# Kernel tuning notes

Hardware: AMD Instinct MI355X
Metric: run time of the kernel (lower is better)

Reference implementation:

```python
import jax, jax.numpy as jnp
import numpy as np

L = 4        # num decoder layers
H = 8        # heads
D = 512      # d_model
DFF = 2048   # ffn hidden
V = 8000     # target vocab
B = 16       # batch
S_ENC = 128  # encoder seq len
T = 32       # decode target_length
START, END, NULL = 1, 2, 0
NEG = -1e9
EPS = 1e-6


def sinusoid_pos(max_len, d):
    pos = np.arange(max_len)[:, None].astype(np.float32)
    i = np.arange(d)[None, :].astype(np.float32)
    ang = pos / np.power(10000.0, (2.0 * np.floor(i / 2.0)) / d)
    pe = np.where(np.arange(d)[None, :] % 2 == 0, np.sin(ang), np.cos(ang))
    return jnp.asarray(pe[None], jnp.float32)  # [1, max_len, d]


def setup_inputs() -> dict:
    key = jax.random.key(0)
    ks = jax.random.split(key, 16)
    g = lambda k, shape: jax.random.normal(k, shape, jnp.float32) * 0.02
    return {
        "target_length": T,
        "encoder_output": jax.random.normal(ks[0], (B, S_ENC, D), jnp.float32),
        "padding_mask": jnp.zeros((B, S_ENC), jnp.float32),  # 1.0 where padded
        "embed": g(ks[1], (V, D)),
        "wq": g(ks[2], (L, D, D)), "wk": g(ks[3], (L, D, D)),
        "wv": g(ks[4], (L, D, D)), "wo": g(ks[5], (L, D, D)),
        "cwq": g(ks[6], (L, D, D)), "cwk": g(ks[7], (L, D, D)),
        "cwv": g(ks[8], (L, D, D)), "cwo": g(ks[9], (L, D, D)),
        "w1": g(ks[10], (L, D, DFF)), "b1": jnp.zeros((L, DFF), jnp.float32),
        "w2": g(ks[11], (L, DFF, D)), "b2": jnp.zeros((L, D), jnp.float32),
        "ln_g": jnp.ones((L, 3, D), jnp.float32), "ln_b": jnp.zeros((L, 3, D), jnp.float32),
        "fc_w": g(ks[12], (D, V)), "fc_b": jnp.zeros((V,), jnp.float32),
    }


def ln(x, g, b):
    m = jnp.mean(x, axis=-1, keepdims=True)
    v = jnp.mean(jnp.square(x - m), axis=-1, keepdims=True)
    return (x - m) * jax.lax.rsqrt(v + EPS) * g + b


def mha(q_in, kv_in, wq, wk, wv, wo, mask):
    Bn, Sq, d = q_in.shape
    dh = d // H
    q = (q_in @ wq).reshape(Bn, Sq, H, dh)
    k = (kv_in @ wk).reshape(Bn, -1, H, dh)
    v = (kv_in @ wv).reshape(Bn, -1, H, dh)
    s = jnp.einsum('bqhd,bkhd->bhqk', q, k) / jnp.sqrt(jnp.float32(dh)) + mask
    a = jax.nn.softmax(s, axis=-1)
    o = jnp.einsum('bhqk,bkhd->bqhd', a, v).reshape(Bn, Sq, d)
    return o @ wo


def decoder_stack(x, encoder_output, self_mask, cross_mask,
                  wq, wk, wv, wo, cwq, cwk, cwv, cwo,
                  w1, b1, w2, b2, ln_g, ln_b):
    for i in range(L):
        a = mha(x, x, wq[i], wk[i], wv[i], wo[i], self_mask)
        x = ln(x + a, ln_g[i, 0], ln_b[i, 0])
        a2 = mha(x, encoder_output, cwq[i], cwk[i], cwv[i], cwo[i], cross_mask)
        x = ln(x + a2, ln_g[i, 1], ln_b[i, 1])
        f = jax.nn.relu(x @ w1[i] + b1[i]) @ w2[i] + b2[i]
        x = ln(x + f, ln_g[i, 2], ln_b[i, 2])
    return x


def reference(target_length, encoder_output, padding_mask, embed,
              wq, wk, wv, wo, cwq, cwk, cwv, cwo,
              w1, b1, w2, b2, ln_g, ln_b, fc_w, fc_b):
    Bn, S, d = encoder_output.shape
    Tp1 = target_length + 1
    pos_enc = sinusoid_pos(Tp1, d)
    sqrt_d = jnp.sqrt(jnp.float32(d))
    cross_mask = padding_mask[:, None, None, :] * NEG  # [B,1,1,S_enc]
    tokens0 = jnp.full((Bn, Tp1), NULL, jnp.int32).at[:, 0].set(START)
    done0 = jnp.zeros((Bn,), bool)

    def step(carry, t):
        tokens, done = carry
        # re-embed the whole (fixed-size, masked) prefix buffer each step
        x = embed[tokens] * sqrt_d + pos_enc
        # only positions <= t are valid keys; no look-ahead mask (matches original)
        self_mask = jnp.where(jnp.arange(Tp1) <= t, 0.0, NEG)[None, None, None, :]
        x = decoder_stack(x, encoder_output, self_mask, cross_mask,
                          wq, wk, wv, wo, cwq, cwk, cwv, cwo,
                          w1, b1, w2, b2, ln_g, ln_b)
        out = x[:, t, :] @ fc_w + fc_b  # logits at last valid position
        max_idx = jnp.argmax(out, axis=-1).astype(jnp.int32)
        done = done | (max_idx == END)
        tok = jnp.where(done, jnp.int32(NULL), max_idx)
        tokens = tokens.at[:, t + 1].set(tok)
        return (tokens, done), None

    (tokens, done), _ = jax.lax.scan(step, (tokens0, done0), jnp.arange(target_length))
    return tokens[:, 1:].astype(jnp.int64)
```

## Files before the change

kernel.cpp:

```cpp
#include <hip/hip_runtime.h>
#include <math.h>

#define L_   4
#define H_   8
#define D_   512
#define DH   64
#define DFF_ 2048
#define V_   8000
#define B_   16
#define SENC 128
#define T_   32
#define TP1  33
#define NEGV -1e9f
#define EPSV 1e-6f
#define SQRTD 22.627416997969522f
#define XSZ  ((size_t)TP1 * B_ * D_)

__global__ __launch_bounds__(256) void gemm32_k(
    const float* __restrict__ A, const float* __restrict__ W,
    const float* __restrict__ bias, float* __restrict__ C,
    int M, int N, int K, int kchunk, size_t pstride, int relu, int tmode)
{
    __shared__ __align__(16) float As[2][16][34];
    __shared__ __align__(16) float Bs[2][16][68];
    int tid = threadIdx.x;
    int tx = tid & 15, ty = tid >> 4;
    int m0 = blockIdx.y * 32, n0 = blockIdx.x * 64;
    int kbeg = blockIdx.z * kchunk;
    int niter = kchunk >> 4;
    C += (size_t)blockIdx.z * pstride;
    int am = tid >> 2, aseg = tid & 3;
    int bk = tid >> 4, bc4 = (tid & 15) * 4;
    float4 aReg = make_float4(0.f, 0.f, 0.f, 0.f), bReg;
    {
        int k0 = kbeg;
        if (tid < 128) {
            int gm = m0 + am;
            if (gm < M) aReg = *(const float4*)&A[(size_t)gm * K + k0 + aseg * 4];
        }
        bReg = *(const float4*)&W[(size_t)(k0 + bk) * N + n0 + bc4];
    }
    if (tid < 128) {
        As[0][aseg * 4 + 0][am] = aReg.x;
        As[0][aseg * 4 + 1][am] = aReg.y;
        As[0][aseg * 4 + 2][am] = aReg.z;
        As[0][aseg * 4 + 3][am] = aReg.w;
    }
    *(float4*)&Bs[0][bk][bc4] = bReg;
    __syncthreads();
    float acc[2][4] = {};
    for (int it = 0; it < niter; it++) {
        int cur = it & 1;
        if (it + 1 < niter) {
            int k0 = kbeg + (it + 1) * 16;
            if (tid < 128) {
                int gm = m0 + am;
                aReg = make_float4(0.f, 0.f, 0.f, 0.f);
                if (gm < M) aReg = *(const float4*)&A[(size_t)gm * K + k0 + aseg * 4];
            }
            bReg = *(const float4*)&W[(size_t)(k0 + bk) * N + n0 + bc4];
        }
        #pragma unroll
        for (int kk = 0; kk < 16; kk++) {
            float2 a2 = *(const float2*)&As[cur][kk][ty * 2];
            float4 b4 = *(const float4*)&Bs[cur][kk][tx * 4];
            acc[0][0] += a2.x * b4.x; acc[0][1] += a2.x * b4.y;
            acc[0][2] += a2.x * b4.z; acc[0][3] += a2.x * b4.w;
            acc[1][0] += a2.y * b4.x; acc[1][1] += a2.y * b4.y;
            acc[1][2] += a2.y * b4.z; acc[1][3] += a2.y * b4.w;
        }
        if (it + 1 < niter) {
            int nxt = 1 - cur;
            if (tid < 128) {
                As[nxt][aseg * 4 + 0][am] = aReg.x;
                As[nxt][aseg * 4 + 1][am] = aReg.y;
                As[nxt][aseg * 4 + 2][am] = aReg.z;
                As[nxt][aseg * 4 + 3][am] = aReg.w;
            }
            *(float4*)&Bs[nxt][bk][bc4] = bReg;
        }
        __syncthreads();
    }
    #pragma unroll
    for (int i = 0; i < 2; i++) {
        int gm = m0 + ty * 2 + i;
        if (gm >= M) continue;
        #pragma unroll
        for (int j = 0; j < 4; j++) {
            int gn = n0 + tx * 4 + j;
            float vv = acc[i][j];
            if (bias) vv += bias[gn];
            if (relu) vv = fmaxf(vv, 0.f);
            if (tmode == 1)
                C[(size_t)(gm >> 7) * 65536 + (size_t)gn * SENC + (gm & 127)] = vv;
            else
                C[(size_t)gm * N + gn] = vv;
        }
    }
}

__global__ __launch_bounds__(256) void gemm_qkv_k(
    const float* __restrict__ A, const float* __restrict__ W0,
    const float* __restrict__ W1, const float* __restrict__ W2,
    float* __restrict__ Cb, int M)
{
    __shared__ __align__(16) float As[2][16][34];
    __shared__ __align__(16) float Bs[2][16][68];
    int sel = blockIdx.x >> 3;
    const float* W = (sel == 0) ? W0 : ((sel == 1) ? W1 : W2);
    float* C = Cb + (size_t)sel * XSZ;
    int tid = threadIdx.x;
    int tx = tid & 15, ty = tid >> 4;
    int m0 = blockIdx.y * 32, n0 = (blockIdx.x & 7) * 64;
    int am = tid >> 2, aseg = tid & 3;
    int bk = tid >> 4, bc4 = (tid & 15) * 4;
    float4 aReg = make_float4(0.f, 0.f, 0.f, 0.f), bReg;
    {
        if (tid < 128) {
            int gm = m0 + am;
            if (gm < M) aReg = *(const float4*)&A[(size_t)gm * D_ + aseg * 4];
        }
        bReg = *(const float4*)&W[(size_t)bk * D_ + n0 + bc4];
    }
    if (tid < 128) {
        As[0][aseg * 4 + 0][am] = aReg.x;
        As[0][aseg * 4 + 1][am] = aReg.y;
        As[0][aseg * 4 + 2][am] = aReg.z;
        As[0][aseg * 4 + 3][am] = aReg.w;
    }
    *(float4*)&Bs[0][bk][bc4] = bReg;
    __syncthreads();
    float acc[2][4] = {};
    for (int it = 0; it < 32; it++) {
        int cur = it & 1;
        if (it + 1 < 32) {
            int k0 = (it + 1) * 16;
            if (tid < 128) {
                int gm = m0 + am;
                aReg = make_float4(0.f, 0.f, 0.f, 0.f);
                if (gm < M) aReg = *(const float4*)&A[(size_t)gm * D_ + k0 + aseg * 4];
            }
            bReg = *(const float4*)&W[(size_t)(k0 + bk) * D_ + n0 + bc4];
        }
        #pragma unroll
        for (int kk = 0; kk < 16; kk++) {
            float2 a2 = *(const float2*)&As[cur][kk][ty * 2];
            float4 b4 = *(const float4*)&Bs[cur][kk][tx * 4];
            acc[0][0] += a2.x * b4.x; acc[0][1] += a2.x * b4.y;
            acc[0][2] += a2.x * b4.z; acc[0][3] += a2.x * b4.w;
            acc[1][0] += a2.y * b4.x; acc[1][1] += a2.y * b4.y;
            acc[1][2] += a2.y * b4.z; acc[1][3] += a2.y * b4.w;
        }
        if (it + 1 < 32) {
            int nxt = 1 - cur;
            if (tid < 128) {
                As[nxt][aseg * 4 + 0][am] = aReg.x;
                As[nxt][aseg * 4 + 1][am] = aReg.y;
                As[nxt][aseg * 4 + 2][am] = aReg.z;
                As[nxt][aseg * 4 + 3][am] = aReg.w;
            }
            *(float4*)&Bs[nxt][bk][bc4] = bReg;
        }
        __syncthreads();
    }
    #pragma unroll
    for (int i = 0; i < 2; i++) {
        int gm = m0 + ty * 2 + i;
        if (gm >= M) continue;
        #pragma unroll
        for (int j = 0; j < 4; j++) {
            int gn = n0 + tx * 4 + j;
            if (sel == 1)
                C[(size_t)(gm & 15) * 16896 + (size_t)gn * TP1 + (gm >> 4)] =
                    acc[i][j];
            else
                C[(size_t)gm * D_ + gn] = acc[i][j];
        }
    }
}

__global__ void init_k(int* __restrict__ tokens, int* __restrict__ done,
                       float* __restrict__ cmask, const float* __restrict__ pm)
{
    int tid = threadIdx.x + blockIdx.x * 256;
    if (tid < B_ * TP1) tokens[tid] = ((tid % TP1) == 0) ? 1 : 0;
    if (tid < B_) done[tid] = 0;
    if (tid < B_ * SENC) cmask[tid] = pm[tid] * NEGV;
}

__global__ __launch_bounds__(256) void pe_k(float* __restrict__ pe)
{
    int p = blockIdx.x;
    for (int d = threadIdx.x; d < D_; d += 256) {
        float fd = (float)(2 * (d / 2)) / (float)D_;
        float ang = (float)p / powf(10000.f, fd);
        pe[(size_t)p * D_ + d] = (d & 1) ? cosf(ang) : sinf(ang);
    }
}

__global__ __launch_bounds__(256) void embed_k(
    const float* __restrict__ embed, int* __restrict__ tokens,
    float* __restrict__ x, const float* __restrict__ pe,
    const float* __restrict__ cand_v, const int* __restrict__ cand_i,
    int* __restrict__ done, int t)
{
    int p = blockIdx.x;
    int b = blockIdx.y;
    int tid = threadIdx.x;
    __shared__ float sv[128];
    __shared__ int si[128];
    __shared__ int stok;
    if (p == t && t > 0) {
        if (tid < 128) {
            float val = -1e30f; int idx = 0x7fffffff;
            if (tid < 125) {
                val = cand_v[(size_t)b * 125 + tid];
                idx = cand_i[(size_t)b * 125 + tid];
            }
            sv[tid] = val; si[tid] = idx;
        }
        __syncthreads();
        for (int s = 64; s; s >>= 1) {
            if (tid < s) {
                float ov = sv[tid + s]; int oi = si[tid + s];
                if (ov > sv[tid] || (ov == sv[tid] && oi < si[tid])) {
                    sv[tid] = ov; si[tid] = oi;
                }
            }
            __syncthreads();
        }
        if (tid == 0) {
            int best = si[0];
            int dn = done[b] | (best == 2 ? 1 : 0);
            done[b] = dn;
            int tk = dn ? 0 : best;
            tokens[b * TP1 + t] = tk;
            stok = tk;
        }
        __syncthreads();
    }
    int tok = (p == t && t > 0) ? stok : tokens[b * TP1 + p];
    const float* e = embed + (size_t)tok * D_;
    const float* pr = pe + (size_t)p * D_;
    float* xr = x + ((size_t)p * B_ + b) * D_;
    int c0 = tid * 2;
    float2 ev = *(const float2*)&e[c0];
    float2 pv = *(const float2*)&pr[c0];
    float2 o;
    o.x = ev.x * SQRTD + pv.x;
    o.y = ev.y * SQRTD + pv.y;
    *(float2*)&xr[c0] = o;
}

__device__ __forceinline__ float block_sum(float s) {
    __shared__ float red[4];
    #pragma unroll
    for (int off = 32; off; off >>= 1) s += __shfl_xor(s, off);
    if ((threadIdx.x & 63) == 0) red[threadIdx.x >> 6] = s;
    __syncthreads();
    float tot = red[0] + red[1] + red[2] + red[3];
    __syncthreads();
    return tot;
}

__device__ __forceinline__ float4 block_sum4(float4 s) {
    __shared__ __align__(16) float red4[4][4];
    #pragma unroll
    for (int off = 32; off; off >>= 1) {
        s.x += __shfl_xor(s.x, off);
        s.y += __shfl_xor(s.y, off);
        s.z += __shfl_xor(s.z, off);
        s.w += __shfl_xor(s.w, off);
    }
    if ((threadIdx.x & 63) == 0) *(float4*)red4[threadIdx.x >> 6] = s;
    __syncthreads();
    float4 t;
    t.x = red4[0][0] + red4[1][0] + red4[2][0] + red4[3][0];
    t.y = red4[0][1] + red4[1][1] + red4[2][1] + red4[3][1];
    t.z = red4[0][2] + red4[1][2] + red4[2][2] + red4[3][2];
    t.w = red4[0][3] + red4[1][3] + red4[2][3] + red4[3][3];
    __syncthreads();
    return t;
}

__global__ __launch_bounds__(256) void attn_mega_k(
    const float* __restrict__ q, const float* __restrict__ kT,
    const float* __restrict__ v, const float* __restrict__ wo,
    const float* __restrict__ KcT, const float* __restrict__ Vc,
    const float* __restrict__ cmask, const float* __restrict__ cwq,
    const float* __restrict__ cwo, float* __restrict__ x,
    const float* __restrict__ lg, const float* __restrict__ lb, int P)
{
    int b = blockIdx.x;
    int p0 = blockIdx.y * 4;
    int tid = threadIdx.x;
    int c0 = tid * 2;
    __shared__ float xs[4][D_];
    __shared__ float arow[4][D_];
    __shared__ float scs[4][H_][SENC + 4];
    __shared__ float inv[4][H_];
    #pragma unroll
    for (int g = 0; g < 4; g++) {
        float2 qv = make_float2(0.f, 0.f);
        if (p0 + g < P)
            qv = *(const float2*)&q[((size_t)(p0 + g) * B_ + b) * D_ + c0];
        *(float2*)&arow[g][c0] = qv;
    }
    __syncthreads();
    {
        int h = tid >> 5, kp = tid & 31;
        float a0 = 0.f, a1 = 0.f, a2 = 0.f, a3 = 0.f;
        if (kp < P) {
            const float* kb = kT + ((size_t)(b * 8 + h) * 64) * TP1 + kp;
            #pragma unroll 8
            for (int d = 0; d < 64; d++) {
                float kv = kb[(size_t)d * TP1];
                a0 += arow[0][h * 64 + d] * kv;
                a1 += arow[1][h * 64 + d] * kv;
                a2 += arow[2][h * 64 + d] * kv;
                a3 += arow[3][h * 64 + d] * kv;
            }
        }
        scs[0][h][kp] = a0 * 0.125f;
        scs[1][h][kp] = a1 * 0.125f;
        scs[2][h][kp] = a2 * 0.125f;
        scs[3][h][kp] = a3 * 0.125f;
    }
    __syncthreads();
    {
        int gh = tid >> 3, lane8 = tid & 7;
        int g = gh >> 3, h = gh & 7;
        float mx = -1e30f;
        for (int j = lane8; j < P; j += 8) mx = fmaxf(mx, scs[g][h][j]);
        mx = fmaxf(mx, __shfl_xor(mx, 1));
        mx = fmaxf(mx, __shfl_xor(mx, 2));
        mx = fmaxf(mx, __shfl_xor(mx, 4));
        float sum = 0.f;
        for (int j = lane8; j < P; j += 8) {
            float e = expf(scs[g][h][j] - mx);
            scs[g][h][j] = e;
            sum += e;
        }
        sum += __shfl_xor(sum, 1);
        sum += __shfl_xor(sum, 2);
        sum += __shfl_xor(sum, 4);
        if (lane8 == 0) inv[g][h] = 1.f / sum;
    }
    __syncthreads();
    {
        int h = tid >> 5;
        float o0[4] = {0.f, 0.f, 0.f, 0.f}, o1[4] = {0.f, 0.f, 0.f, 0.f};
        for (int j = 0; j < P; j++) {
            float2 vv = *(const float2*)&v[((size_t)j * B_ + b) * D_ + c0];
            #pragma unroll
            for (int g = 0; g < 4; g++) {
                float w = scs[g][h][j];
                o0[g] += w * vv.x; o1[g] += w * vv.y;
            }
        }
        #pragma unroll
        for (int g = 0; g < 4; g++) {
            arow[g][c0]     = o0[g] * inv[g][h];
            arow[g][c0 + 1] = o1[g] * inv[g][h];
        }
    }
    __syncthreads();
    {
        float v0[4], v1[4];
        #pragma unroll
        for (int g = 0; g < 4; g++) {
            float2 xv = make_float2(0.f, 0.f);
            if (p0 + g < P)
                xv = *(const float2*)&x[((size_t)(p0 + g) * B_ + b) * D_ + c0];
            v0[g] = xv.x; v1[g] = xv.y;
        }
        #pragma unroll 8
        for (int k = 0; k < D_; k++) {
            float2 wv = *(const float2*)&wo[(size_t)k * D_ + c0];
            #pragma unroll
            for (int g = 0; g < 4; g++) {
                float a = arow[g][k];
                v0[g] += a * wv.x; v1[g] += a * wv.y;
            }
// ... 65 lines not shown
    __syncthreads();
    {
        int gh = tid >> 3, lane8 = tid & 7;
        int g = gh >> 3, h = gh & 7;
        float mx = -1e30f;
        for (int s = lane8; s < SENC; s += 8) mx = fmaxf(mx, scs[g][h][s]);
        mx = fmaxf(mx, __shfl_xor(mx, 1));
        mx = fmaxf(mx, __shfl_xor(mx, 2));
        mx = fmaxf(mx, __shfl_xor(mx, 4));
        float sum = 0.f;
        for (int s = lane8; s < SENC; s += 8) {
            float e = expf(scs[g][h][s] - mx);
            scs[g][h][s] = e;
            sum += e;
        }
        sum += __shfl_xor(sum, 1);
        sum += __shfl_xor(sum, 2);
        sum += __shfl_xor(sum, 4);
        if (lane8 == 0) inv[g][h] = 1.f / sum;
    }
    __syncthreads();
    {
        int h = tid >> 5;
        float o0[4] = {0.f, 0.f, 0.f, 0.f}, o1[4] = {0.f, 0.f, 0.f, 0.f};
        for (int s = 0; s < SENC; s++) {
            float2 vv = *(const float2*)&Vc[((size_t)b * SENC + s) * D_ + c0];
            #pragma unroll
            for (int g = 0; g < 4; g++) {
                float w = scs[g][h][s];
                o0[g] += w * vv.x; o1[g] += w * vv.y;
            }
        }
        #pragma unroll
        for (int g = 0; g < 4; g++) {
            arow[g][c0]     = o0[g] * inv[g][h];
            arow[g][c0 + 1] = o1[g] * inv[g][h];
        }
    }
    __syncthreads();
    {
        float v0[4], v1[4];
        #pragma unroll
        for (int g = 0; g < 4; g++) {
            v0[g] = xs[g][c0]; v1[g] = xs[g][c0 + 1];
        }
        #pragma unroll 8
        for (int k = 0; k < D_; k++) {
            float2 wv = *(const float2*)&cwo[(size_t)k * D_ + c0];
            #pragma unroll
            for (int g = 0; g < 4; g++) {
                float a = arow[g][k];
                v0[g] += a * wv.x; v1[g] += a * wv.y;
            }
        }
        float4 s1 = make_float4(v0[0] + v1[0], v0[1] + v1[1],
                                v0[2] + v1[2], v0[3] + v1[3]);
        float4 m4 = block_sum4(s1);
        float mean[4] = {m4.x * (1.f / 512.f), m4.y * (1.f / 512.f),
                         m4.z * (1.f / 512.f), m4.w * (1.f / 512.f)};
        float d0[4], d1[4];
        #pragma unroll
        for (int g = 0; g < 4; g++) {
            d0[g] = v0[g] - mean[g]; d1[g] = v1[g] - mean[g];
        }
        float4 s2 = make_float4(d0[0] * d0[0] + d1[0] * d1[0],
                                d0[1] * d0[1] + d1[1] * d1[1],
                                d0[2] * d0[2] + d1[2] * d1[2],
                                d0[3] * d0[3] + d1[3] * d1[3]);
        float4 w4 = block_sum4(s2);
        float var[4] = {w4.x * (1.f / 512.f), w4.y * (1.f / 512.f),
                        w4.z * (1.f / 512.f), w4.w * (1.f / 512.f)};
        float g0 = lg[D_ + c0], g1 = lg[D_ + c0 + 1];
        float bb0 = lb[D_ + c0], bb1 = lb[D_ + c0 + 1];
        #pragma unroll
        for (int g = 0; g < 4; g++) {
            if (p0 + g < P) {
                float rs = rsqrtf(var[g] + EPSV);
                float* xr = x + ((size_t)(p0 + g) * B_ + b) * D_;
                xr[c0]     = d0[g] * rs * g0 + bb0;
                xr[c0 + 1] = d1[g] * rs * g1 + bb1;
            }
        }
    }
}

__global__ __launch_bounds__(256) void ln_red_k(
    float* __restrict__ x, const float* __restrict__ parts, size_t pstride,
    int nparts, const float* __restrict__ bias,
    const float* __restrict__ gam, const float* __restrict__ bet)
{
    int r = blockIdx.x;
    float* xr = x + (size_t)r * D_;
    int tid = threadIdx.x;
    float v0 = xr[tid];
    float v1 = xr[tid + 256];
    for (int s = 0; s < nparts; s++) {
        const float* pr = parts + (size_t)s * pstride + (size_t)r * D_;
        v0 += pr[tid];
        v1 += pr[tid + 256];
    }
    if (bias) { v0 += bias[tid]; v1 += bias[tid + 256]; }
    float mean = block_sum(v0 + v1) * (1.f / 512.f);
    float d0 = v0 - mean, d1 = v1 - mean;
    float var = block_sum(d0 * d0 + d1 * d1) * (1.f / 512.f);
    float rs = rsqrtf(var + EPSV);
    xr[tid]       = d0 * rs * gam[tid] + bet[tid];
    xr[tid + 256] = d1 * rs * gam[tid + 256] + bet[tid + 256];
}

__global__ __launch_bounds__(256) void logits_k(
    const float* __restrict__ x, const float* __restrict__ fcw,
    const float* __restrict__ fcb, float* __restrict__ cand_v,
    int* __restrict__ cand_i, int t)
{
    __shared__ float xs[B_][D_];
    __shared__ float red[4][64][B_];
    int tid = threadIdx.x;
    for (int i = tid; i < B_ * D_; i += 256) {
        int b = i >> 9, d = i & 511;
        xs[b][d] = x[((size_t)t * B_ + b) * D_ + d];
    }
    __syncthreads();
    int lane = tid & 63, ks = tid >> 6;
    int col = blockIdx.x * 64 + lane;
    float acc[B_] = {};
    int kb = ks * 128;
    for (int k = kb; k < kb + 128; k++) {
        float w = fcw[(size_t)k * V_ + col];
        #pragma unroll
        for (int b = 0; b < B_; b++) acc[b] += xs[b][k] * w;
    }
    #pragma unroll
    for (int b = 0; b < B_; b++) red[ks][lane][b] = acc[b];
    __syncthreads();
    if (ks == 0) {
        float bias = fcb[col];
        #pragma unroll
        for (int b = 0; b < B_; b++) {
            float val = red[0][lane][b] + red[1][lane][b]
                      + red[2][lane][b] + red[3][lane][b] + bias;
            int idx = col;
            #pragma unroll
            for (int off = 32; off; off >>= 1) {
                float ov = __shfl_down(val, off);
                int oi = __shfl_down(idx, off);
                if (ov > val || (ov == val && oi < idx)) { val = ov; idx = oi; }
            }
            if (lane == 0) {
                cand_v[(size_t)b * 125 + blockIdx.x] = val;
                cand_i[(size_t)b * 125 + blockIdx.x] = idx;
            }
        }
    }
}

__global__ __launch_bounds__(128) void writeout_k(
    const int* __restrict__ tokens, const float* __restrict__ cand_v,
    const int* __restrict__ cand_i, const int* __restrict__ done,
    int* __restrict__ out)
{
    int b = blockIdx.x;
    int tid = threadIdx.x;
    __shared__ float sv[128];
    __shared__ int si[128];
    __shared__ int stok;
    float val = -1e30f; int idx = 0x7fffffff;
    if (tid < 125) {
        val = cand_v[(size_t)b * 125 + tid];
        idx = cand_i[(size_t)b * 125 + tid];
    }
    sv[tid] = val; si[tid] = idx;
    __syncthreads();
    for (int s = 64; s; s >>= 1) {
        if (tid < s) {
            float ov = sv[tid + s]; int oi = si[tid + s];
            if (ov > sv[tid] || (ov == sv[tid] && oi < si[tid])) {
                sv[tid] = ov; si[tid] = oi;
            }
        }
        __syncthreads();
    }
    if (tid == 0) {
        int best = si[0];
        int dn = done[b] | (best == 2 ? 1 : 0);
        stok = dn ? 0 : best;
    }
    __syncthreads();
    if (tid < T_)
        out[b * T_ + tid] = (tid == T_ - 1) ? stok : tokens[b * TP1 + tid + 1];
}

extern "C" void kernel_launch(void* const* d_in, const int* in_sizes, int n_in,
                              void* d_out, int out_size, void* d_ws, size_t ws_size,
                              hipStream_t stream)
{
    const float* enc   = (const float*)d_in[1];
    const float* pm    = (const float*)d_in[2];
    const float* embed = (const float*)d_in[3];
    const float* wq    = (const float*)d_in[4];
    const float* wk    = (const float*)d_in[5];
    const float* wv    = (const float*)d_in[6];
    const float* wo    = (const float*)d_in[7];
    const float* cwq   = (const float*)d_in[8];
    const float* cwk   = (const float*)d_in[9];
    const float* cwv   = (const float*)d_in[10];
    const float* cwo   = (const float*)d_in[11];
    const float* w1    = (const float*)d_in[12];
    const float* b1    = (const float*)d_in[13];
    const float* w2    = (const float*)d_in[14];
    const float* b2    = (const float*)d_in[15];
    const float* ln_g  = (const float*)d_in[16];
    const float* ln_b  = (const float*)d_in[17];
    const float* fcw   = (const float*)d_in[18];
    const float* fcb   = (const float*)d_in[19];

    float* ws = (float*)d_ws;
    size_t off = 0;
    float* x     = ws + off; off += XSZ;
    float* qkv   = ws + off; off += 3 * XSZ;
    float* parts = ws + off; off += 4 * XSZ;
    float* ffnh  = ws + off; off += (size_t)TP1 * B_ * DFF_;
    float* cand_v= ws + off; off += (size_t)B_ * 125;
    float* KcT   = ws + off; off += (size_t)L_ * B_ * SENC * D_;
    float* Vc    = ws + off; off += (size_t)L_ * B_ * SENC * D_;
    float* cmask = ws + off; off += (size_t)B_ * SENC;
    float* pe    = ws + off; off += (size_t)TP1 * D_;
    int* cand_i  = (int*)(ws + off); off += (size_t)B_ * 125;
    int* tokens  = (int*)(ws + off); off += (B_ * TP1 + 63) & ~63;
    int* done    = (int*)(ws + off); off += 64;

    init_k<<<8, 256, 0, stream>>>(tokens, done, cmask, pm);
    pe_k<<<TP1, 256, 0, stream>>>(pe);

    const size_t KVL = (size_t)B_ * SENC * D_;
    for (int l = 0; l < L_; l++) {
        gemm32_k<<<dim3(8, (B_ * SENC) / 32), 256, 0, stream>>>(
            enc, cwk + (size_t)l * D_ * D_, nullptr, KcT + l * KVL,
            B_ * SENC, D_, D_, D_, 0, 0, 1);
        gemm32_k<<<dim3(8, (B_ * SENC) / 32), 256, 0, stream>>>(
            enc, cwv + (size_t)l * D_ * D_, nullptr, Vc + l * KVL,
            B_ * SENC, D_, D_, D_, 0, 0, 0);
    }

    for (int t = 0; t < T_; t++) {
        int P = t + 1;
        int M = P * B_;
        int mt = (M + 31) / 32;

        embed_k<<<dim3(P, B_), 256, 0, stream>>>(
            embed, tokens, x, pe, cand_v, cand_i, done, t);

        for (int l = 0; l < L_; l++) {
            const size_t lw = (size_t)l * D_ * D_;
            gemm_qkv_k<<<dim3(24, mt), 256, 0, stream>>>(
                x, wq + lw, wk + lw, wv + lw, qkv, M);
            attn_mega_k<<<dim3(B_, (P + 3) / 4), 256, 0, stream>>>(
                qkv, qkv + XSZ, qkv + 2 * XSZ, wo + lw,
                KcT + l * KVL, Vc + l * KVL, cmask, cwq + lw, cwo + lw, x,
                ln_g + (size_t)(l * 3 + 0) * D_, ln_b + (size_t)(l * 3 + 0) * D_, P);
            gemm32_k<<<dim3(32, mt), 256, 0, stream>>>(
                x, w1 + (size_t)l * D_ * DFF_, b1 + (size_t)l * DFF_, ffnh,
                M, DFF_, D_, D_, 0, 1, 0);
            gemm32_k<<<dim3(8, mt, 4), 256, 0, stream>>>(
                ffnh, w2 + (size_t)l * DFF_ * D_, nullptr, parts,
                M, D_, DFF_, 512, XSZ, 0, 0);
            ln_red_k<<<M, 256, 0, stream>>>(x, parts, XSZ, 4, b2 + (size_t)l * D_,
                ln_g + (size_t)(l * 3 + 2) * D_, ln_b + (size_t)(l * 3 + 2) * D_);
        }

        logits_k<<<V_ / 64, 256, 0, stream>>>(x, fcw, fcb, cand_v, cand_i, t);
    }

    writeout_k<<<B_, 128, 0, stream>>>(tokens, cand_v, cand_i, done, (int*)d_out);
}
```

Before: 24.24 ms.

## Fuse whole decode loop into one persistent cooperative kernel with grid barriers

Replaces the roughly 800 separate kernel launches (embed, qkv, attention, FFN, layernorm, logits per step and layer) with a single persistent cooperative kernel of 256 blocks. The blocks loop over the same tiles and separate stages with an atomic-counter grid barrier. The goal is to remove launch overhead and inter-kernel gaps, which dominate because each step has small M. The cost is a spin barrier per stage and 48KB of static shared memory per block, which may limit occupancy. If the cooperative launch fails, the original multi-kernel path is kept as a fallback.

Result: slower. 84.92 ms (+250.3%).

```diff
diff --git a/kernel.cpp b/kernel.cpp
--- a/kernel.cpp
+++ b/kernel.cpp
@@ -15,20 +15,69 @@
 #define EPSV 1e-6f
 #define SQRTD 22.627416997969522f
 #define XSZ  ((size_t)TP1 * B_ * D_)
-
-__global__ __launch_bounds__(256) void gemm32_k(
+#define NB   256
+
+__device__ __forceinline__ float block_sum(float s) {
+    __shared__ float red[4];
+    #pragma unroll
+    for (int off = 32; off; off >>= 1) s += __shfl_xor(s, off);
+    if ((threadIdx.x & 63) == 0) red[threadIdx.x >> 6] = s;
+    __syncthreads();
+    float tot = red[0] + red[1] + red[2] + red[3];
+    __syncthreads();
+    return tot;
+}
+
+__device__ __forceinline__ float4 block_sum4(float4 s) {
+    __shared__ __align__(16) float red4[4][4];
+    #pragma unroll
+    for (int off = 32; off; off >>= 1) {
+        s.x += __shfl_xor(s.x, off);
+        s.y += __shfl_xor(s.y, off);
+        s.z += __shfl_xor(s.z, off);
+        s.w += __shfl_xor(s.w, off);
+    }
+    if ((threadIdx.x & 63) == 0) *(float4*)red4[threadIdx.x >> 6] = s;
+    __syncthreads();
+    float4 t;
+    t.x = red4[0][0] + red4[1][0] + red4[2][0] + red4[3][0];
+    t.y = red4[0][1] + red4[1][1] + red4[2][1] + red4[3][1];
+    t.z = red4[0][2] + red4[1][2] + red4[2][2] + red4[3][2];
+    t.w = red4[0][3] + red4[1][3] + red4[2][3] + red4[3][3];
+    __syncthreads();
+    return t;
+}
+
+__device__ __forceinline__ void gsync(unsigned* bar, unsigned& gen)
+{
+    __syncthreads();
+    if (threadIdx.x == 0) {
+        __threadfence();
+        atomicAdd(bar, 1u);
+        gen += NB;
+        while (__hip_atomic_load(bar, __ATOMIC_RELAXED,
+                                 __HIP_MEMORY_SCOPE_AGENT) < gen)
+            __builtin_amdgcn_s_sleep(4);
+        __threadfence();
+    }
+    __syncthreads();
+}
+
+
+__device__ void gemm_tile(
     const float* __restrict__ A, const float* __restrict__ W,
     const float* __restrict__ bias, float* __restrict__ C,
-    int M, int N, int K, int kchunk, size_t pstride, int relu, int tmode)
-{
-    __shared__ __align__(16) float As[2][16][34];
-    __shared__ __align__(16) float Bs[2][16][68];
+    int M, int N, int K, int kchunk, size_t pstride, int relu, int tmode,
+    int bx, int by, int bz, float* smem)
+{
+    float (*As)[16][34] = (float (*)[16][34])smem;
+    float (*Bs)[16][68] = (float (*)[16][68])(smem + 1088);
     int tid = threadIdx.x;
     int tx = tid & 15, ty = tid >> 4;
-    int m0 = blockIdx.y * 32, n0 = blockIdx.x * 64;
-    int kbeg = blockIdx.z * kchunk;
+    int m0 = by * 32, n0 = bx * 64;
+    int kbeg = bz * kchunk;
     int niter = kchunk >> 4;
-    C += (size_t)blockIdx.z * pstride;
+    C += (size_t)bz * pstride;
     int am = tid >> 2, aseg = tid & 3;
     int bk = tid >> 4, bc4 = (tid & 15) * 4;
     float4 aReg = make_float4(0.f, 0.f, 0.f, 0.f), bReg;
@@ -99,19 +148,19 @@
     }
 }
 
-__global__ __launch_bounds__(256) void gemm_qkv_k(
+__device__ void qkv_tile(
     const float* __restrict__ A, const float* __restrict__ W0,
     const float* __restrict__ W1, const float* __restrict__ W2,
-    float* __restrict__ Cb, int M)
-{
-    __shared__ __align__(16) float As[2][16][34];
-    __shared__ __align__(16) float Bs[2][16][68];
-    int sel = blockIdx.x >> 3;
+    float* __restrict__ Cb, int M, int bx, int by, float* smem)
+{
+    float (*As)[16][34] = (float (*)[16][34])smem;
+    float (*Bs)[16][68] = (float (*)[16][68])(smem + 1088);
+    int sel = bx >> 3;
     const float* W = (sel == 0) ? W0 : ((sel == 1) ? W1 : W2);
     float* C = Cb + (size_t)sel * XSZ;
     int tid = threadIdx.x;
     int tx = tid & 15, ty = tid >> 4;
-    int m0 = blockIdx.y * 32, n0 = (blockIdx.x & 7) * 64;
+    int m0 = by * 32, n0 = (bx & 7) * 64;
     int am = tid >> 2, aseg = tid & 3;
     int bk = tid >> 4, bc4 = (tid & 15) * 4;
     float4 aReg = make_float4(0.f, 0.f, 0.f, 0.f), bReg;
@@ -179,126 +228,21 @@
     }
 }
 
-__global__ void init_k(int* __restrict__ tokens, int* __restrict__ done,
-                       float* __restrict__ cmask, const float* __restrict__ pm)
-{
-    int tid = threadIdx.x + blockIdx.x * 256;
-    if (tid < B_ * TP1) tokens[tid] = ((tid % TP1) == 0) ? 1 : 0;
-    if (tid < B_) done[tid] = 0;
-    if (tid < B_ * SENC) cmask[tid] = pm[tid] * NEGV;
-}
-
-__global__ __launch_bounds__(256) void pe_k(float* __restrict__ pe)
-{
-    int p = blockIdx.x;
-    for (int d = threadIdx.x; d < D_; d += 256) {
-        float fd = (float)(2 * (d / 2)) / (float)D_;
-        float ang = (float)p / powf(10000.f, fd);
-        pe[(size_t)p * D_ + d] = (d & 1) ? cosf(ang) : sinf(ang);
-    }
-}
-
-__global__ __launch_bounds__(256) void embed_k(
-    const float* __restrict__ embed, int* __restrict__ tokens,
-    float* __restrict__ x, const float* __restrict__ pe,
-    const float* __restrict__ cand_v, const int* __restrict__ cand_i,
-    int* __restrict__ done, int t)
-{
-    int p = blockIdx.x;
-    int b = blockIdx.y;
-    int tid = threadIdx.x;
-    __shared__ float sv[128];
-    __shared__ int si[128];
-    __shared__ int stok;
-    if (p == t && t > 0) {
-        if (tid < 128) {
-            float val = -1e30f; int idx = 0x7fffffff;
-            if (tid < 125) {
-                val = cand_v[(size_t)b * 125 + tid];
-                idx = cand_i[(size_t)b * 125 + tid];
-            }
-            sv[tid] = val; si[tid] = idx;
-        }
-        __syncthreads();
-        for (int s = 64; s; s >>= 1) {
-            if (tid < s) {
-                float ov = sv[tid + s]; int oi = si[tid + s];
-                if (ov > sv[tid] || (ov == sv[tid] && oi < si[tid])) {
-                    sv[tid] = ov; si[tid] = oi;
-                }
-            }
-            __syncthreads();
-        }
-        if (tid == 0) {
-            int best = si[0];
-            int dn = done[b] | (best == 2 ? 1 : 0);
-            done[b] = dn;
-            int tk = dn ? 0 : best;
-            tokens[b * TP1 + t] = tk;
-            stok = tk;
-        }
-        __syncthreads();
-    }
-    int tok = (p == t && t > 0) ? stok : tokens[b * TP1 + p];
-    const float* e = embed + (size_t)tok * D_;
-    const float* pr = pe + (size_t)p * D_;
-    float* xr = x + ((size_t)p * B_ + b) * D_;
-    int c0 = tid * 2;
-    float2 ev = *(const float2*)&e[c0];
-    float2 pv = *(const float2*)&pr[c0];
-    float2 o;
-    o.x = ev.x * SQRTD + pv.x;
-    o.y = ev.y * SQRTD + pv.y;
-    *(float2*)&xr[c0] = o;
-}
-
-__device__ __forceinline__ float block_sum(float s) {
-    __shared__ float red[4];
-    #pragma unroll
-    for (int off = 32; off; off >>= 1) s += __shfl_xor(s, off);
-    if ((threadIdx.x & 63) == 0) red[threadIdx.x >> 6] = s;
-    __syncthreads();
-    float tot = red[0] + red[1] + red[2] + red[3];
-    __syncthreads();
-    return tot;
-}
-
-__device__ __forceinline__ float4 block_sum4(float4 s) {
-    __shared__ __align__(16) float red4[4][4];
-    #pragma unroll
-    for (int off = 32; off; off >>= 1) {
-        s.x += __shfl_xor(s.x, off);
-        s.y += __shfl_xor(s.y, off);
-        s.z += __shfl_xor(s.z, off);
-        s.w += __shfl_xor(s.w, off);
-    }
-    if ((threadIdx.x & 63) == 0) *(float4*)red4[threadIdx.x >> 6] = s;
-    __syncthreads();
-    float4 t;
-    t.x = red4[0][0] + red4[1][0] + red4[2][0] + red4[3][0];
-    t.y = red4[0][1] + red4[1][1] + red4[2][1] + red4[3][1];
-    t.z = red4[0][2] + red4[1][2] + red4[2][2] + red4[3][2];
-    t.w = red4[0][3] + red4[1][3] + red4[2][3] + red4[3][3];
-    __syncthreads();
-    return t;
-}
-
-__global__ __launch_bounds__(256) void attn_mega_k(
+__device__ void attn_tile(
     const float* __restrict__ q, const float* __restrict__ kT,
     const float* __restrict__ v, const float* __restrict__ wo,
     const float* __restrict__ KcT, const float* __restrict__ Vc,
     const float* __restrict__ cmask, const float* __restrict__ cwq,
     const float* __restrict__ cwo, float* __restrict__ x,
-    const float* __restrict__ lg, const float* __restrict__ lb, int P)
-{
-    int b = blockIdx.x;
-    int p0 = blockIdx.y * 4;
+    const float* __restrict__ lg, const float* __restrict__ lb,
+    int P, int b, int p0, float* smem)
+{
+    float (*xs)[D_]            = (float (*)[D_])smem;
+    float (*arow)[D_]          = (float (*)[D_])(smem + 2048);
+    float (*scs)[H_][SENC + 4] = (float (*)[H_][SENC + 4])(smem + 4096);
+    float (*inv)[H_]           = (float (*)[H_])(smem + 8320);
     int tid = threadIdx.x;
     int c0 = tid * 2;
-    __shared__ float xs[4][D_];
-    __shared__ float arow[4][D_];
-    __shared__ float scs[4][H_][SENC + 4];
-    __shared__ float inv[4][H_];
     #pragma unroll
     for (int g = 0; g < 4; g++) {
         float2 qv = make_float2(0.f, 0.f);
@@ -530,14 +474,14 @@
             }
         }
     }
-}
-
-__global__ __launch_bounds__(256) void ln_red_k(
+    __syncthreads();
+}
+
+__device__ void ln_row(
     float* __restrict__ x, const float* __restrict__ parts, size_t pstride,
     int nparts, const float* __restrict__ bias,
-    const float* __restrict__ gam, const float* __restrict__ bet)
-{
-    int r = blockIdx.x;
+    const float* __restrict__ gam, const float* __restrict__ bet, int r)
+{
     float* xr = x + (size_t)r * D_;
     int tid = threadIdx.x;
     float v0 = xr[tid];
@@ -556,13 +500,13 @@
     xr[tid + 256] = d1 * rs * gam[tid + 256] + bet[tid + 256];
 }
 
-__global__ __launch_bounds__(256) void logits_k(
+__device__ void logits_tile(
     const float* __restrict__ x, const float* __restrict__ fcw,
     const float* __restrict__ fcb, float* __restrict__ cand_v,
-    int* __restrict__ cand_i, int t)
-{
-    __shared__ float xs[B_][D_];
-    __shared__ float red[4][64][B_];
+    int* __restrict__ cand_i, int t, int bx, float* smem)
+{
+    float (*xs)[D_]      = (float (*)[D_])smem;
+    float (*red)[64][B_] = (float (*)[64][B_])(smem + 8192);
     int tid = threadIdx.x;
     for (int i = tid; i < B_ * D_; i += 256) {
         int b = i >> 9, d = i & 511;
@@ -570,7 +514,7 @@
     }
     __syncthreads();
     int lane = tid & 63, ks = tid >> 6;
-    int col = blockIdx.x * 64 + lane;
+    int col = bx * 64 + lane;
     float acc[B_] = {};
     int kb = ks * 128;
     for (int k = kb; k < kb + 128; k++) {
@@ -595,32 +539,87 @@
                 if (ov > val || (ov == val && oi < idx)) { val = ov; idx = oi; }
             }
             if (lane == 0) {
-                cand_v[(size_t)b * 125 + blockIdx.x] = val;
-                cand_i[(size_t)b * 125 + blockIdx.x] = idx;
-            }
-        }
-    }
-}
-
-__global__ __launch_bounds__(128) void writeout_k(
+                cand_v[(size_t)b * 125 + bx] = val;
+                cand_i[(size_t)b * 125 + bx] = idx;
+            }
+        }
+    }
+    __syncthreads();
+}
+
+__device__ void embed_item(
+    const float* __restrict__ embed, int* __restrict__ tokens,
+    float* __restrict__ x, const float* __restrict__ pe,
+    const float* __restrict__ cand_v, const int* __restrict__ cand_i,
+    int* __restrict__ done, int t, int p, int b, float* smem)
+{
+    float* sv = smem;
+    int* si   = (int*)(smem + 128);
+    int* stok = (int*)(smem + 256);
+    int tid = threadIdx.x;
+    if (p == t && t > 0) {
+        if (tid < 128) {
+            float val = -1e30f; int idx = 0x7fffffff;
+            if (tid < 125) {
+                val = cand_v[(size_t)b * 125 + tid];
+                idx = cand_i[(size_t)b * 125 + tid];
+            }
+            sv[tid] = val; si[tid] = idx;
+        }
+        __syncthreads();
+        for (int s = 64; s; s >>= 1) {
+            if (tid < s) {
+                float ov = sv[tid + s]; int oi = si[tid + s];
+                if (ov > sv[tid] || (ov == sv[tid] && oi < si[tid])) {
+                    sv[tid] = ov; si[tid] = oi;
+                }
+            }
+            __syncthreads();
+        }
+        if (tid == 0) {
+            int best = si[0];
+            int dn = done[b] | (best == 2 ? 1 : 0);
+            done[b] = dn;
+            int tk = dn ? 0 : best;
+            tokens[b * TP1 + t] = tk;
+            *stok = tk;
+        }
+        __syncthreads();
+    }
+    int tok = (p == t && t > 0) ? *stok : tokens[b * TP1 + p];
+    const float* e = embed + (size_t)tok * D_;
+    const float* pr = pe + (size_t)p * D_;
+    float* xr = x + ((size_t)p * B_ + b) * D_;
+    int c0 = tid * 2;
+    float2 ev = *(const float2*)&e[c0];
+    float2 pv = *(const float2*)&pr[c0];
+    float2 o;
+    o.x = ev.x * SQRTD + pv.x;
+    o.y = ev.y * SQRTD + pv.y;
+    *(float2*)&xr[c0] = o;
+    __syncthreads();
+}
+
+__device__ void writeout_item(
     const int* __restrict__ tokens, const float* __restrict__ cand_v,
     const int* __restrict__ cand_i, const int* __restrict__ done,
-    int* __restrict__ out)
-{
-    int b = blockIdx.x;
+    int* __restrict__ out, int b, float* smem)
+{
+    float* sv = smem;
+    int* si   = (int*)(smem + 128);
+    int* stok = (int*)(smem + 256);
     int tid = threadIdx.x;
-    __shared__ float sv[128];
-    __shared__ int si[128];
-    __shared__ int stok;
-    float val = -1e30f; int idx = 0x7fffffff;
-    if (tid < 125) {
-        val = cand_v[(size_t)b * 125 + tid];
-        idx = cand_i[(size_t)b * 125 + tid];
-    }
-    sv[tid] = val; si[tid] = idx;
+    if (tid < 128) {
+        float val = -1e30f; int idx = 0x7fffffff;
+        if (tid < 125) {
+            val = cand_v[(size_t)b * 125 + tid];
+            idx = cand_i[(size_t)b * 125 + tid];
+        }
+        sv[tid] = val; si[tid] = idx;
+    }
     __syncthreads();
     for (int s = 64; s; s >>= 1) {
-        if (tid < s) {
+        if (tid < s && tid < 128) {
             float ov = sv[tid + s]; int oi = si[tid + s];
             if (ov > sv[tid] || (ov == sv[tid] && oi < si[tid])) {
                 sv[tid] = ov; si[tid] = oi;
@@ -631,11 +630,186 @@
     if (tid == 0) {
         int best = si[0];
         int dn = done[b] | (best == 2 ? 1 : 0);
-        stok = dn ? 0 : best;
+        *stok = dn ? 0 : best;
     }
     __syncthreads();
     if (tid < T_)
-        out[b * T_ + tid] = (tid == T_ - 1) ? stok : tokens[b * TP1 + tid + 1];
+        out[b * T_ + tid] = (tid == T_ - 1) ? *stok : tokens[b * TP1 + tid + 1];
+    __syncthreads();
+}
+
+struct MegaParams {
+    const float *enc, *pm, *embed;
+    const float *wq, *wk, *wv, *wo, *cwq, *cwk, *cwv, *cwo;
+    const float *w1, *b1, *w2, *b2, *ln_g, *ln_b, *fcw, *fcb;
+    float *x, *qkv, *parts, *ffnh, *cand_v, *KcT, *Vc, *cmask, *pe;
+    int *cand_i, *tokens, *done, *out;
+    unsigned *bar;
+};
+
+__global__ __launch_bounds__(256) void mega_k(MegaParams mp)
+{
+    __shared__ __align__(16) float smem[12288];
+    const int bid = blockIdx.x;
+    const int tid = threadIdx.x;
+    unsigned gen = 0;
+    const size_t KVL = (size_t)B_ * SENC * D_;
+
+    for (int i = bid * 256 + tid; i < TP1 * D_; i += NB * 256) {
+        int p = i / D_, d = i % D_;
+        float fd = (float)(2 * (d / 2)) / (float)D_;
+        float ang = (float)p / powf(10000.f, fd);
+        mp.pe[i] = (d & 1) ? cosf(ang) : sinf(ang);
+        if (i < B_ * TP1) mp.tokens[i] = ((i % TP1) == 0) ? 1 : 0;
+        if (i < B_) mp.done[i] = 0;
+        if (i < B_ * SENC) mp.cmask[i] = mp.pm[i] * NEGV;
+    }
+    __syncthreads();
+    for (int tile = bid; tile < 8 * 512; tile += NB) {
+        int g = tile >> 9, sub = tile & 511;
+        int l = g >> 1, kv = g & 1;
+        int bx = sub & 7, by = sub >> 3;
+        if (kv == 0)
+            gemm_tile(mp.enc, mp.cwk + (size_t)l * D_ * D_, nullptr,
+                      mp.KcT + (size_t)l * KVL, B_ * SENC, D_, D_, D_, 0, 0, 1,
+                      bx, by, 0, smem);
+        else
+            gemm_tile(mp.enc, mp.cwv + (size_t)l * D_ * D_, nullptr,
+                      mp.Vc + (size_t)l * KVL, B_ * SENC, D_, D_, D_, 0, 0, 0,
+                      bx, by, 0, smem);
+    }
+    gsync(mp.bar, gen);
+
+    for (int t = 0; t < T_; t++) {
+        int P = t + 1, M = P * B_, mt = (M + 31) >> 5;
+
+        for (int item = bid; item < M; item += NB)
+            embed_item(mp.embed, mp.tokens, mp.x, mp.pe, mp.cand_v, mp.cand_i,
+                       mp.done, t, item >> 4, item & 15, smem);
+        gsync(mp.bar, gen);
+
+        for (int l = 0; l < L_; l++) {
+            const size_t lw = (size_t)l * D_ * D_;
+
+            for (int tile = bid; tile < 24 * mt; tile += NB)
+                qkv_tile(mp.x, mp.wq + lw, mp.wk + lw, mp.wv + lw, mp.qkv, M,
+                         tile % 24, tile / 24, smem);
+            gsync(mp.bar, gen);
+
+            int pt = (P + 3) >> 2;
+            for (int tile = bid; tile < 16 * pt; tile += NB)
+                attn_tile(mp.qkv, mp.qkv + XSZ, mp.qkv + 2 * XSZ, mp.wo + lw,
+                          mp.KcT + (size_t)l * KVL, mp.Vc + (size_t)l * KVL,
+                          mp.cmask, mp.cwq + lw, mp.cwo + lw, mp.x,
+                          mp.ln_g + (size_t)(l * 3 + 0) * D_,
+                          mp.ln_b + (size_t)(l * 3 + 0) * D_,
+                          P, tile & 15, (tile >> 4) * 4, smem);
+            gsync(mp.bar, gen);
+
+            for (int tile = bid; tile < 32 * mt; tile += NB)
+                gemm_tile(mp.x, mp.w1 + (size_t)l * D_ * DFF_,
+                          mp.b1 + (size_t)l * DFF_, mp.ffnh,
+                          M, DFF_, D_, D_, 0, 1, 0, tile % 32, tile / 32, 0, smem);
+            gsync(mp.bar, gen);
+
+            for (int tile = bid; tile < 8 * mt * 4; tile += NB) {
+                int bx = tile % 8, rest = tile / 8;
+                gemm_tile(mp.ffnh, mp.w2 + (size_t)l * DFF_ * D_, nullptr,
+                          mp.parts, M, D_, DFF_, 512, XSZ, 0, 0,
+                          bx, rest % mt, rest / mt, smem);
+            }
+            gsync(mp.bar, gen);
+
+            for (int r = bid; r < M; r += NB)
+                ln_row(mp.x, mp.parts, XSZ, 4, mp.b2 + (size_t)l * D_,
+                       mp.ln_g + (size_t)(l * 3 + 2) * D_,
+                       mp.ln_b + (size_t)(l * 3 + 2) * D_, r);
+            gsync(mp.bar, gen);
+        }
+
+        for (int tile = bid; tile < V_ / 64; tile += NB)
+            logits_tile(mp.x, mp.fcw, mp.fcb, mp.cand_v, mp.cand_i, t, tile, smem);
+        gsync(mp.bar, gen);
+    }
+
+    for (int b = bid; b < B_; b += NB)
+        writeout_item(mp.tokens, mp.cand_v, mp.cand_i, mp.done, mp.out, b, smem);
+}
+
+__global__ void barinit_k(unsigned* bar) { if (threadIdx.x == 0) *bar = 0u; }
+
+__global__ __launch_bounds__(256) void gemm32_k(
+    const float* A, const float* W, const float* bias, float* C,
+    int M, int N, int K, int kchunk, size_t pstride, int relu, int tmode)
+{
+    __shared__ __align__(16) float smem[3264];
+    gemm_tile(A, W, bias, C, M, N, K, kchunk, pstride, relu, tmode,
+              blockIdx.x, blockIdx.y, blockIdx.z, smem);
+}
+
+__global__ __launch_bounds__(256) void gemm_qkv_k(
+    const float* A, const float* W0, const float* W1, const float* W2,
+    float* Cb, int M)
+{
+    __shared__ __align__(16) float smem[3264];
+    qkv_tile(A, W0, W1, W2, Cb, M, blockIdx.x, blockIdx.y, smem);
+}
+
+__global__ __launch_bounds__(256) void attn_mega_k(
+    const float* q, const float* kT, const float* v, const float* wo,
+    const float* KcT, const float* Vc, const float* cmask, const float* cwq,
+    const float* cwo, float* x, const float* lg, const float* lb, int P)
+{
+    __shared__ __align__(16) float smem[8352];
+    attn_tile(q, kT, v, wo, KcT, Vc, cmask, cwq, cwo, x, lg, lb,
+              P, blockIdx.x, blockIdx.y * 4, smem);
+}
+
+__global__ __launch_bounds__(256) void ln_red_k(
+    float* x, const float* parts, size_t pstride, int nparts,
+    const float* bias, const float* gam, const float* bet)
+{
+    ln_row(x, parts, pstride, nparts, bias, gam, bet, blockIdx.x);
+}
+
+__global__ __launch_bounds__(256) void logits_k(
+    const float* x, const float* fcw, const float* fcb,
+    float* cand_v, int* cand_i, int t)
+{
+    __shared__ __align__(16) float smem[12288];
+    logits_tile(x, fcw, fcb, cand_v, cand_i, t, blockIdx.x, smem);
+}
+
+__global__ __launch_bounds__(256) void embed_k(
+    const float* embed, int* tokens, float* x, const float* pe,
+    const float* cand_v, const int* cand_i, int* done, int t)
+{
+    __shared__ __align__(16) float smem[264];
+    embed_item(embed, tokens, x, pe, cand_v, cand_i, done, t,
+               blockIdx.x, blockIdx.y, smem);
+}
+
+__global__ __launch_bounds__(256) void initpe_k(
+    int* tokens, int* done, float* cmask, const float* pm, float* pe)
+{
+    for (int i = blockIdx.x * 256 + threadIdx.x; i < TP1 * D_;
+         i += gridDim.x * 256) {
+        int p = i / D_, d = i % D_;
+        float fd = (float)(2 * (d / 2)) / (float)D_;
+        float ang = (float)p / powf(10000.f, fd);
+        pe[i] = (d & 1) ? cosf(ang) : sinf(ang);
+        if (i < B_ * TP1) tokens[i] = ((i % TP1) == 0) ? 1 : 0;
+        if (i < B_) done[i] = 0;
+        if (i < B_ * SENC) cmask[i] = pm[i] * NEGV;
+    }
+}
+
+__global__ __launch_bounds__(256) void writeout_k(
+    const int* tokens, const float* cand_v, const int* cand_i,
+    const int* done, int* out)
+{
+    __shared__ __align__(16) float smem[264];
+    writeout_item(tokens, cand_v, cand_i, done, out, blockIdx.x, smem);
 }
 
 extern "C" void kernel_launch(void* const* d_in, const int* in_sizes, int n_in,
@@ -644,7 +818,7 @@
 {
     const float* enc   = (const float*)d_in[1];
     const float* pm    = (const float*)d_in[2];
-    const float* embed = (const float*)d_in[3];
+    const float* embd  = (const float*)d_in[3];
     const float* wq    = (const float*)d_in[4];
     const float* wk    = (const float*)d_in[5];
     const float* wv    = (const float*)d_in[6];
@@ -676,10 +850,26 @@
     int* cand_i  = (int*)(ws + off); off += (size_t)B_ * 125;
     int* tokens  = (int*)(ws + off); off += (B_ * TP1 + 63) & ~63;
     int* done    = (int*)(ws + off); off += 64;
-
-    init_k<<<8, 256, 0, stream>>>(tokens, done, cmask, pm);
-    pe_k<<<TP1, 256, 0, stream>>>(pe);
-
+    unsigned* bar= (unsigned*)(ws + off); off += 64;
+
+    barinit_k<<<1, 64, 0, stream>>>(bar);
+    MegaParams mp;
+    mp.enc = enc;  mp.pm = pm;  mp.embed = embd;
+    mp.wq = wq;    mp.wk = wk;  mp.wv = wv;  mp.wo = wo;
+    mp.cwq = cwq;  mp.cwk = cwk; mp.cwv = cwv; mp.cwo = cwo;
+    mp.w1 = w1;    mp.b1 = b1;  mp.w2 = w2;  mp.b2 = b2;
+    mp.ln_g = ln_g; mp.ln_b = ln_b; mp.fcw = fcw; mp.fcb = fcb;
+    mp.x = x;      mp.qkv = qkv; mp.parts = parts; mp.ffnh = ffnh;
+    mp.cand_v = cand_v; mp.KcT = KcT; mp.Vc = Vc; mp.cmask = cmask;
+    mp.pe = pe;    mp.cand_i = cand_i; mp.tokens = tokens; mp.done = done;
+    mp.out = (int*)d_out; mp.bar = bar;
+    void* kargs[] = { (void*)&mp };
+    hipError_t err = hipLaunchCooperativeKernel(
+        (const void*)mega_k, dim3(NB), dim3(256), kargs, 0, stream);
+    if (err == hipSuccess) return;
+
+    (void)hipGetLastError();
+    initpe_k<<<66, 256, 0, stream>>>(tokens, done, cmask, pm, pe);
     const size_t KVL = (size_t)B_ * SENC * D_;
     for (int l = 0; l < L_; l++) {
         gemm32_k<<<dim3(8, (B_ * SENC) / 32), 256, 0, stream>>>(
@@ -689,15 +879,12 @@
             enc, cwv + (size_t)l * D_ * D_, nullptr, Vc + l * KVL,
             B_ * SENC, D_, D_, D_, 0, 0, 0);
     }
-
     for (int t = 0; t < T_; t++) {
         int P = t + 1;
         int M = P * B_;
         int mt = (M + 31) / 32;
-
         embed_k<<<dim3(P, B_), 256, 0, stream>>>(
-            embed, tokens, x, pe, cand_v, cand_i, done, t);
-
+            embd, tokens, x, pe, cand_v, cand_i, done, t);
         for (int l = 0; l < L_; l++) {
             const size_t lw = (size_t)l * D_ * D_;
             gemm_qkv_k<<<dim3(24, mt), 256, 0, stream>>>(
@@ -715,9 +902,7 @@
             ln_red_k<<<M, 256, 0, stream>>>(x, parts, XSZ, 4, b2 + (size_t)l * D_,
                 ln_g + (size_t)(l * 3 + 2) * D_, ln_b + (size_t)(l * 3 + 2) * D_);
         }
-
         logits_k<<<V_ / 64, 256, 0, stream>>>(x, fcw, fcb, cand_v, cand_i, t);
     }
-
     writeout_k<<<B_, 128, 0, stream>>>(tokens, cand_v, cand_i, done, (int*)d_out);
 }
```

## Fuse FFN up-projection, ReLU and down-projection into one kernel per chunk

Applied to the files above, without the earlier changes.

Adds a kernel where each block computes a 128-wide slice of the FFN hidden layer for 16 rows, keeps the bias+ReLU result in shared memory, and multiplies it straight into W2 to write a partial sum. The 16 partials are then summed by the existing residual/layernorm reduction kernel. This removes the global round trip of the hidden activation and one launch per layer. In exchange the partial buffer grows, the reduction reads 16 partials instead of 4, and the block has only 16 output columns of parallelism in the second stage. The new path is taken only when the workspace is large enough; otherwise the old path runs.

New measurement: 23.60 ms. 2.6% less time.

```diff
diff --git a/kernel.cpp b/kernel.cpp
--- a/kernel.cpp
+++ b/kernel.cpp
@@ -15,6 +15,7 @@
 #define EPSV 1e-6f
 #define SQRTD 22.627416997969522f
 #define XSZ  ((size_t)TP1 * B_ * D_)
+#define NCH  16
 
 __global__ __launch_bounds__(256) void gemm32_k(
     const float* __restrict__ A, const float* __restrict__ W,
@@ -175,6 +176,112 @@
                     acc[i][j];
             else
                 C[(size_t)gm * D_ + gn] = acc[i][j];
+        }
+    }
+}
+
+__global__ __launch_bounds__(256) void ffn_fused_k(
+    const float* __restrict__ A, const float* __restrict__ w1,
+    const float* __restrict__ b1, const float* __restrict__ w2,
+    float* __restrict__ parts, int M)
+{
+    __shared__ __align__(16) float As[2][16][18];
+    __shared__ __align__(16) float Bs[2][16][132];
+    __shared__ __align__(16) float hs[16][132];
+    int tid = threadIdx.x;
+    int bx = blockIdx.x;
+    int r0 = blockIdx.y * 16;
+    int ty = tid >> 5, tx = tid & 31;
+    int am = tid >> 2, aseg = tid & 3;
+    int bk = tid >> 4, bc4 = (tid & 15) * 4;
+    const float* W1c = w1 + bx * 128;
+    float4 aReg = make_float4(0.f, 0.f, 0.f, 0.f), bReg0, bReg1;
+    {
+        if (tid < 64) {
+            int gm = r0 + am;
+            if (gm < M) aReg = *(const float4*)&A[(size_t)gm * D_ + aseg * 4];
+        }
+        bReg0 = *(const float4*)&W1c[(size_t)bk * DFF_ + bc4];
+        bReg1 = *(const float4*)&W1c[(size_t)bk * DFF_ + bc4 + 64];
+    }
+    if (tid < 64) {
+        As[0][aseg * 4 + 0][am] = aReg.x;
+        As[0][aseg * 4 + 1][am] = aReg.y;
+        As[0][aseg * 4 + 2][am] = aReg.z;
+        As[0][aseg * 4 + 3][am] = aReg.w;
+    }
+    *(float4*)&Bs[0][bk][bc4]      = bReg0;
+    *(float4*)&Bs[0][bk][bc4 + 64] = bReg1;
+    __syncthreads();
+    float acc[2][4] = {};
+    for (int it = 0; it < 32; it++) {
+        int cur = it & 1;
+        if (it + 1 < 32) {
+            int k0 = (it + 1) * 16;
+            if (tid < 64) {
+                int gm = r0 + am;
+                aReg = make_float4(0.f, 0.f, 0.f, 0.f);
+                if (gm < M) aReg = *(const float4*)&A[(size_t)gm * D_ + k0 + aseg * 4];
+            }
+            bReg0 = *(const float4*)&W1c[(size_t)(k0 + bk) * DFF_ + bc4];
+            bReg1 = *(const float4*)&W1c[(size_t)(k0 + bk) * DFF_ + bc4 + 64];
+        }
+        #pragma unroll
+        for (int kk = 0; kk < 16; kk++) {
+            float2 a2 = *(const float2*)&As[cur][kk][ty * 2];
+            float4 b4 = *(const float4*)&Bs[cur][kk][tx * 4];
+            acc[0][0] += a2.x * b4.x; acc[0][1] += a2.x * b4.y;
+            acc[0][2] += a2.x * b4.z; acc[0][3] += a2.x * b4.w;
+            acc[1][0] += a2.y * b4.x; acc[1][1] += a2.y * b4.y;
+            acc[1][2] += a2.y * b4.z; acc[1][3] += a2.y * b4.w;
+        }
+        if (it + 1 < 32) {
+            int nxt = 1 - cur;
+            if (tid < 64) {
+                As[nxt][aseg * 4 + 0][am] = aReg.x;
+                As[nxt][aseg * 4 + 1][am] = aReg.y;
+                As[nxt][aseg * 4 + 2][am] = aReg.z;
+                As[nxt][aseg * 4 + 3][am] = aReg.w;
+            }
+            *(float4*)&Bs[nxt][bk][bc4]      = bReg0;
+            *(float4*)&Bs[nxt][bk][bc4 + 64] = bReg1;
+        }
+        __syncthreads();
+    }
+    {
+        float4 bv = *(const float4*)&b1[bx * 128 + tx * 4];
+        #pragma unroll
+        for (int i = 0; i < 2; i++) {
+            float4 o;
+            o.x = fmaxf(acc[i][0] + bv.x, 0.f);
+            o.y = fmaxf(acc[i][1] + bv.y, 0.f);
+            o.z = fmaxf(acc[i][2] + bv.z, 0.f);
+            o.w = fmaxf(acc[i][3] + bv.w, 0.f);
+            *(float4*)&hs[ty * 2 + i][tx * 4] = o;
+        }
+    }
+    __syncthreads();
+    int rh = tid >> 7, cg = tid & 127;
+    float acc2[8][4] = {};
+    const float* W2c = w2 + (size_t)(bx * 128) * D_;
+    for (int k = 0; k < 128; k++) {
+        float4 w4 = *(const float4*)&W2c[(size_t)k * D_ + cg * 4];
+        #pragma unroll
+        for (int r = 0; r < 8; r++) {
+            float h = hs[rh * 8 + r][k];
+            acc2[r][0] += h * w4.x; acc2[r][1] += h * w4.y;
+            acc2[r][2] += h * w4.z; acc2[r][3] += h * w4.w;
+        }
+    }
+    float* P = parts + (size_t)bx * XSZ;
+    #pragma unroll
+    for (int r = 0; r < 8; r++) {
+        int gm = r0 + rh * 8 + r;
+        if (gm < M) {
+            float4 o;
+            o.x = acc2[r][0]; o.y = acc2[r][1];
+            o.z = acc2[r][2]; o.w = acc2[r][3];
+            *(float4*)&P[(size_t)gm * D_ + cg * 4] = o;
         }
     }
 }
@@ -666,8 +773,8 @@
     size_t off = 0;
     float* x     = ws + off; off += XSZ;
     float* qkv   = ws + off; off += 3 * XSZ;
-    float* parts = ws + off; off += 4 * XSZ;
-    float* ffnh  = ws + off; off += (size_t)TP1 * B_ * DFF_;
+    float* parts = ws + off; off += NCH * XSZ;
+    float* ffnh  = parts + 4 * XSZ;
     float* cand_v= ws + off; off += (size_t)B_ * 125;
     float* KcT   = ws + off; off += (size_t)L_ * B_ * SENC * D_;
     float* Vc    = ws + off; off += (size_t)L_ * B_ * SENC * D_;
@@ -676,6 +783,7 @@
     int* cand_i  = (int*)(ws + off); off += (size_t)B_ * 125;
     int* tokens  = (int*)(ws + off); off += (B_ * TP1 + 63) & ~63;
     int* done    = (int*)(ws + off); off += 64;
+    int fused = (ws_size >= off * sizeof(float)) ? 1 : 0;
 
     init_k<<<8, 256, 0, stream>>>(tokens, done, cmask, pm);
     pe_k<<<TP1, 256, 0, stream>>>(pe);
@@ -706,14 +814,24 @@
                 qkv, qkv + XSZ, qkv + 2 * XSZ, wo + lw,
                 KcT + l * KVL, Vc + l * KVL, cmask, cwq + lw, cwo + lw, x,
                 ln_g + (size_t)(l * 3 + 0) * D_, ln_b + (size_t)(l * 3 + 0) * D_, P);
-            gemm32_k<<<dim3(32, mt), 256, 0, stream>>>(
-                x, w1 + (size_t)l * D_ * DFF_, b1 + (size_t)l * DFF_, ffnh,
-                M, DFF_, D_, D_, 0, 1, 0);
-            gemm32_k<<<dim3(8, mt, 4), 256, 0, stream>>>(
-                ffnh, w2 + (size_t)l * DFF_ * D_, nullptr, parts,
-                M, D_, DFF_, 512, XSZ, 0, 0);
-            ln_red_k<<<M, 256, 0, stream>>>(x, parts, XSZ, 4, b2 + (size_t)l * D_,
-                ln_g + (size_t)(l * 3 + 2) * D_, ln_b + (size_t)(l * 3 + 2) * D_);
+            if (fused) {
+                ffn_fused_k<<<dim3(NCH, (M + 15) / 16), 256, 0, stream>>>(
+                    x, w1 + (size_t)l * D_ * DFF_, b1 + (size_t)l * DFF_,
+                    w2 + (size_t)l * DFF_ * D_, parts, M);
+                ln_red_k<<<M, 256, 0, stream>>>(x, parts, XSZ, NCH,
+                    b2 + (size_t)l * D_,
+                    ln_g + (size_t)(l * 3 + 2) * D_, ln_b + (size_t)(l * 3 + 2) * D_);
+            } else {
+                gemm32_k<<<dim3(32, mt), 256, 0, stream>>>(
+                    x, w1 + (size_t)l * D_ * DFF_, b1 + (size_t)l * DFF_, ffnh,
+                    M, DFF_, D_, D_, 0, 1, 0);
+                gemm32_k<<<dim3(8, mt, 4), 256, 0, stream>>>(
+                    ffnh, w2 + (size_t)l * DFF_ * D_, nullptr, parts,
+                    M, D_, DFF_, 512, XSZ, 0, 0);
+                ln_red_k<<<M, 256, 0, stream>>>(x, parts, XSZ, 4,
+                    b2 + (size_t)l * D_,
+                    ln_g + (size_t)(l * 3 + 2) * D_, ln_b + (size_t)(l * 3 + 2) * D_);
+            }
         }
 
         logits_k<<<V_ / 64, 256, 0, stream>>>(x, fcw, fcb, cand_v, cand_i, t);
```
